# Optimization experiments

Hardware: AMD Instinct MI355X
Metric: run time of the kernel (lower is better)

The kernel has to match this reference:

```python
import jax, jax.numpy as jnp
import numpy as np

WS, SS, P, H = 7, 3, 14, 12  # window, shift, patch grid, heads
NW = (P // WS) ** 2          # windows per image = 4
N_WIN = WS * WS              # tokens per window = 49

def _rel_pos_index():
    coords = np.stack(np.meshgrid(np.arange(WS), np.arange(WS), indexing='ij')).reshape(2, -1)
    rel = (coords[:, :, None] - coords[:, None, :]).transpose(1, 2, 0).astype(np.int64)
    rel[..., 0] += WS - 1
    rel[..., 1] += WS - 1
    rel[..., 0] *= 2 * WS - 1
    return rel.sum(-1)  # [49,49]

def _shift_mask():
    img = np.zeros((P, P))
    sl = (slice(0, -WS), slice(-WS, -SS), slice(-SS, None))
    cnt = 0
    for h in sl:
        for w in sl:
            img[h, w] = cnt
            cnt += 1
    mw = img.reshape(P // WS, WS, P // WS, WS).transpose(0, 2, 1, 3).reshape(-1, N_WIN)
    am = mw[:, None, :] - mw[:, :, None]
    return np.where(am != 0, -100.0, 0.0).astype(np.float32)  # [nW,49,49]

RPI = jnp.asarray(_rel_pos_index())
MASK = jnp.asarray(_shift_mask())

def _hswish(x):
    return x * jnp.clip(x + 3.0, 0.0, 6.0) / 6.0

def _hsig(x):
    return jnp.clip(x + 3.0, 0.0, 6.0) / 6.0

def _bn(x, g, b, eps=1e-5):
    # training-mode batchnorm over (B,H,W) per channel, biased variance
    m = x.mean((0, 2, 3), keepdims=True)
    v = ((x - m) ** 2).mean((0, 2, 3), keepdims=True)
    return (x - m) / jnp.sqrt(v + eps) * g[None, :, None, None] + b[None, :, None, None]

def setup_inputs() -> dict:
    key = jax.random.key(0)
    ks = jax.random.split(key, 20)
    C, HID = 768, 3072
    return {
        'x': jax.random.normal(ks[0], (32, 197, C), jnp.float32),
        'w_qkv': jax.random.normal(ks[1], (3 * C, C), jnp.float32) * 0.02,
        'w_proj': jax.random.normal(ks[2], (C, C), jnp.float32) * 0.02,
        'b_proj': jax.random.normal(ks[3], (C,), jnp.float32) * 0.02,
        'rpb_table': jax.random.normal(ks[4], ((2 * WS - 1) ** 2, H), jnp.float32) * 0.02,
        'pw1_w': jax.random.normal(ks[5], (HID, C), jnp.float32) * 0.02,
        'bn1_g': 1.0 + jax.random.normal(ks[6], (HID,), jnp.float32) * 0.02,
        'bn1_b': jax.random.normal(ks[7], (HID,), jnp.float32) * 0.02,
        'dw_w': jax.random.normal(ks[8], (HID, 3, 3), jnp.float32) * 0.1,
        'bn2_g': 1.0 + jax.random.normal(ks[9], (HID,), jnp.float32) * 0.02,
        'bn2_b': jax.random.normal(ks[10], (HID,), jnp.float32) * 0.02,
        'se_w1': jax.random.normal(ks[11], (HID // 4, HID), jnp.float32) * 0.02,
        'se_b1': jax.random.normal(ks[12], (HID // 4,), jnp.float32) * 0.02,
        'se_w2': jax.random.normal(ks[13], (HID, HID // 4), jnp.float32) * 0.02,
        'se_b2': jax.random.normal(ks[14], (HID,), jnp.float32) * 0.02,
        'pw2_w': jax.random.normal(ks[15], (C, HID), jnp.float32) * 0.02,
        'bn3_g': 1.0 + jax.random.normal(ks[16], (C,), jnp.float32) * 0.02,
        'bn3_b': jax.random.normal(ks[17], (C,), jnp.float32) * 0.02,
    }

def reference(x, w_qkv, w_proj, b_proj, rpb_table, pw1_w, bn1_g, bn1_b, dw_w,
              bn2_g, bn2_b, se_w1, se_b1, se_w2, se_b2, pw2_w, bn3_g, bn3_b):
    B, N, C = x.shape
    hd = C // H
    scale = hd ** -0.5
    nw = P // WS

    cls_tok = x[:, :1]
    xs = x[:, 1:].reshape(B, P, P, C)
    xs = jnp.roll(xs, (-SS, -SS), axis=(1, 2))  # cyclic shift
    # window partition -> [B*nW, 49, C]
    win = xs.reshape(B, nw, WS, nw, WS, C).transpose(0, 1, 3, 2, 4, 5).reshape(B * NW, N_WIN, C)

    qkv = (win @ w_qkv.T).reshape(B * NW, N_WIN, 3, H, hd).transpose(2, 0, 3, 1, 4)
    q, k, v = qkv[0], qkv[1], qkv[2]  # [B*nW, H, 49, hd]
    attn = jnp.einsum('bhqd,bhkd->bhqk', q, k) * scale
    # relative position bias gather: [H,49,49]
    bias = rpb_table[RPI.reshape(-1)].reshape(N_WIN, N_WIN, H).transpose(2, 0, 1)
    attn = attn + bias[None]
    # shifted-window mask add
    attn = (attn.reshape(B, NW, H, N_WIN, N_WIN) + MASK[None, :, None]).reshape(B * NW, H, N_WIN, N_WIN)
    attn = jax.nn.softmax(attn, axis=-1)
    out = jnp.einsum('bhqk,bhkd->bhqd', attn, v).transpose(0, 2, 1, 3).reshape(B * NW, N_WIN, C)
    out = out @ w_proj.T + b_proj

    # window reverse + reverse shift
    xs = out.reshape(B, nw, nw, WS, WS, C).transpose(0, 1, 3, 2, 4, 5).reshape(B, P, P, C)
    xs = jnp.roll(xs, (SS, SS), axis=(1, 2))
    x = jnp.concatenate([cls_tok, xs.reshape(B, P * P, C)], axis=1)

    # LocalityFeedForward (inverted residual conv MLP with SE)
    cls_tok, xt = x[:, :1], x[:, 1:]
    f = xt.transpose(0, 2, 1).reshape(B, C, P, P)
    h = _hswish(_bn(jnp.einsum('bchw,oc->bohw', f, pw1_w), bn1_g, bn1_b))
    h = _hswish(_bn(jax.lax.conv_general_dilated(
        h, dw_w[:, None], (1, 1), 'SAME',
        feature_group_count=h.shape[1],
        dimension_numbers=('NCHW', 'OIHW', 'NCHW')), bn2_g, bn2_b))
    s = h.mean((2, 3))  # global avg pool [B, hid]
    s = _hsig(jax.nn.relu(s @ se_w1.T + se_b1) @ se_w2.T + se_b2)
    h = h * s[:, :, None, None]
    h = _bn(jnp.einsum('bchw,oc->bohw', h, pw2_w), bn3_g, bn3_b)
    f = f + h
    x = jnp.concatenate([cls_tok, f.reshape(B, C, P * P).transpose(0, 2, 1)], axis=1)
    return x
```

## Files before the change

### kernel.cpp

```cpp
#include <hip/hip_runtime.h>
#include <hip/hip_bf16.h>

typedef unsigned short ushort_t;
typedef unsigned int uint_t;
typedef short short8 __attribute__((ext_vector_type(8)));
typedef float floatx4 __attribute__((ext_vector_type(4)));

__device__ inline float b2f(ushort_t u){
    uint_t v = ((uint_t)u) << 16;
    return __uint_as_float(v);
}
__device__ inline ushort_t f2b(float f){
    uint_t v = __float_as_uint(f);
    uint_t r = (v + 0x7FFFu + ((v >> 16) & 1u)) >> 16;
    return (ushort_t)r;
}
__device__ inline void unpack8(uint4 u, float* f){
    uint_t w[4] = {u.x, u.y, u.z, u.w};
    #pragma unroll
    for (int i = 0; i < 4; ++i){
        f[2*i]   = __uint_as_float(w[i] << 16);
        f[2*i+1] = __uint_as_float(w[i] & 0xFFFF0000u);
    }
}
__device__ inline uint4 pack8(const float* f){
    uint4 o;
    uint_t w[4];
    #pragma unroll
    for (int i = 0; i < 4; ++i)
        w[i] = (uint_t)f2b(f[2*i]) | ((uint_t)f2b(f[2*i+1]) << 16);
    o.x = w[0]; o.y = w[1]; o.z = w[2]; o.w = w[3];
    return o;
}
__device__ inline ushort4 cvt4(float4 v){
    ushort4 o;
    o.x = f2b(v.x); o.y = f2b(v.y); o.z = f2b(v.z); o.w = f2b(v.w);
    return o;
}
__device__ inline float hswish(float y){
    return y * fminf(fmaxf(y + 3.f, 0.f), 6.f) * (1.f/6.f);
}

#define MROWS 6272
#define CDIM  768
#define HID   3072
#define QKV3  2304

__device__ inline int scatter_row(int ri){
    int w  = ri / 49, t = ri % 49;
    int b  = w >> 2,  wi = w & 3;
    int wy = wi >> 1, wx = wi & 1;
    int ty = t / 7,   tx = t % 7;
    int yd = (wy*7 + ty + 3) % 14;
    int xd = (wx*7 + tx + 3) % 14;
    return b*196 + yd*14 + xd;
}

__global__ __launch_bounds__(256) void cvt_f2b(const float4* __restrict__ in,
                                               ushort4* __restrict__ out, int n4){
    int i = blockIdx.x * 256 + threadIdx.x;
    if (i < n4) out[i] = cvt4(in[i]);
}

__global__ __launch_bounds__(256) void dw_transpose(const float* __restrict__ w,
                                                    float* __restrict__ wT){
    int i = blockIdx.x*256 + threadIdx.x;
    if (i < HID*9){ int c = i/9, k = i%9; wT[k*HID + c] = w[i]; }
}

__global__ __launch_bounds__(256) void gather_win(const float4* __restrict__ x,
                                                  ushort4* __restrict__ win){
    int idx = blockIdx.x * 256 + threadIdx.x;
    if (idx >= MROWS * 192) return;
    int r  = idx / 192, c4 = idx % 192;
    int w  = r / 49,  t  = r % 49;
    int b  = w >> 2,  wi = w & 3;
    int wy = wi >> 1, wx = wi & 1;
    int ty = t / 7,   tx = t % 7;
    int ys = (wy*7 + ty + 3) % 14;
    int xs = (wx*7 + tx + 3) % 14;
    win[idx] = cvt4(x[(size_t)b*197*192 + (size_t)(1 + ys*14 + xs)*192 + c4]);
}

__global__ __launch_bounds__(256) void gemm_bt(const ushort_t* __restrict__ A,
                                               const ushort_t* __restrict__ B,
                                               ushort_t* __restrict__ Cb,
                                               float* __restrict__ Cf,
                                               int M, int N, int K,
                                               const float* __restrict__ bias,
                                               float* __restrict__ stats,
                                               int scat){
    const int nx   = gridDim.x;
    int flat = blockIdx.y * nx + blockIdx.x;
    int xcd  = flat & 7;
    int k    = flat >> 3;
    int by   = xcd + 8 * (k / nx);
    int bx   = k % nx;
    if (by * 128 >= M) return;

    __shared__ __align__(16) ushort_t As[2][128*32];
    __shared__ __align__(16) ushort_t Bs[2][128*32];
    const int tid  = threadIdx.x;
    const int lane = tid & 63;
    const int wid  = tid >> 6;
    const int m0 = by * 128;
    const int n0 = bx * 128;
    const int wm = (wid >> 1) * 64;
    const int wn = (wid & 1) * 64;

    const int srow = (lane >> 2);
    const int scol = (lane & 3) * 8;

    floatx4 acc[4][4] = {};

    auto stage = [&](int buf, int k0){
        #pragma unroll
        for (int j = 0; j < 2; ++j){
            int ch  = wid*2 + j;
            const ushort_t* gA = A + (size_t)(m0 + ch*16 + srow)*K + k0 + scol;
            const ushort_t* gB = B + (size_t)(n0 + ch*16 + srow)*K + k0 + scol;
            __builtin_amdgcn_global_load_lds(
                (const __attribute__((address_space(1))) void*)gA,
                (__attribute__((address_space(3))) void*)(&As[buf][ch*512 + lane*8]), 16, 0, 0);
            __builtin_amdgcn_global_load_lds(
                (const __attribute__((address_space(1))) void*)gB,
                (__attribute__((address_space(3))) void*)(&Bs[buf][ch*512 + lane*8]), 16, 0, 0);
        }
    };

    stage(0, 0);
    __syncthreads();

    int cur = 0;
    const int fr = lane & 15;
    const int co = (lane >> 4) * 8;
    for (int k0 = 0; k0 < K; k0 += 32){
        if (k0 + 32 < K) stage(cur ^ 1, k0 + 32);

        short8 af[4], bfr[4];
        #pragma unroll
        for (int i = 0; i < 4; ++i){
            af[i]  = *(const short8*)(&As[cur][(wm + i*16 + fr)*32 + co]);
            bfr[i] = *(const short8*)(&Bs[cur][(wn + i*16 + fr)*32 + co]);
        }
        #pragma unroll
        for (int i = 0; i < 4; ++i)
            #pragma unroll
            for (int j = 0; j < 4; ++j)
                acc[i][j] = __builtin_amdgcn_mfma_f32_16x16x32_bf16(af[i], bfr[j], acc[i][j], 0, 0, 0);

        __syncthreads();
        cur ^= 1;
    }

    #pragma unroll
    for (int i = 0; i < 4; ++i){
        int grow = m0 + wm + i*16 + (lane >> 4)*4;
        #pragma unroll
        for (int j = 0; j < 4; ++j){
            int gcol = n0 + wn + j*16 + (lane & 15);
            float bv = bias ? bias[gcol] : 0.f;
            if (scat){
                #pragma unroll
                for (int r = 0; r < 4; ++r){
                    float v = acc[i][j][r] + bv;
                    size_t off = (size_t)scatter_row(grow + r)*N + gcol;
                    Cf[off] = v;
                    Cb[off] = f2b(v);
                }
            } else if (Cb){
                #pragma unroll
                for (int r = 0; r < 4; ++r)
                    Cb[(size_t)(grow + r)*N + gcol] = f2b(acc[i][j][r] + bv);
            } else {
                #pragma unroll
                for (int r = 0; r < 4; ++r)
                    Cf[(size_t)(grow + r)*N + gcol] = acc[i][j][r] + bv;
            }
        }
    }

    if (stats){
        #pragma unroll
        for (int j = 0; j < 4; ++j){
            int gcol = n0 + wn + j*16 + (lane & 15);
            float bv = bias ? bias[gcol] : 0.f;
            float sv = 0.f, sq = 0.f;
            #pragma unroll
            for (int i = 0; i < 4; ++i)
                #pragma unroll
                for (int r = 0; r < 4; ++r){
                    float v = acc[i][j][r] + bv;
                    sv += v; sq += v*v;
                }
            sv += __shfl_xor(sv, 16, 64);  sq += __shfl_xor(sq, 16, 64);
            sv += __shfl_xor(sv, 32, 64);  sq += __shfl_xor(sq, 32, 64);
            if (lane < 16){
                atomicAdd(&stats[gcol], sv);
                atomicAdd(&stats[N + gcol], sq);
            }
        }
    }
}

__global__ __launch_bounds__(256) void gemm_bt64(const ushort_t* __restrict__ A,
                                                 const ushort_t* __restrict__ B,
                                                 ushort_t* __restrict__ Cb,
                                                 float* __restrict__ Cf,
                                                 int M, int N, int K,
                                                 const float* __restrict__ bias,
                                                 float* __restrict__ stats,
                                                 int scat){
    const int nx   = gridDim.x;
    int flat = blockIdx.y * nx + blockIdx.x;
    int xcd  = flat & 7;
    int k    = flat >> 3;
    int by   = xcd + 8 * (k / nx);
    int bx   = k % nx;
    if (by * 128 >= M) return;

    __shared__ __align__(16) ushort_t As[2][128*32];
    __shared__ __align__(16) ushort_t Bs[2][64*32];
    const int tid  = threadIdx.x;
    const int lane = tid & 63;
    const int wid  = tid >> 6;
    const int m0 = by * 128;
    const int n0 = bx * 64;
    const int wm = (wid >> 1) * 64;
    const int wn = (wid & 1) * 32;

    const int srow = (lane >> 2);
    const int scol = (lane & 3) * 8;

    floatx4 acc[4][2] = {};

    auto stage = [&](int buf, int k0){
        #pragma unroll
        for (int j = 0; j < 2; ++j){
            int ch = wid*2 + j;
            const ushort_t* gA = A + (size_t)(m0 + ch*16 + srow)*K + k0 + scol;
            __builtin_amdgcn_global_load_lds(
                (const __attribute__((address_space(1))) void*)gA,
                (__attribute__((address_space(3))) void*)(&As[buf][ch*512 + lane*8]), 16, 0, 0);
        }
        const ushort_t* gB = B + (size_t)(n0 + wid*16 + srow)*K + k0 + scol;
        __builtin_amdgcn_global_load_lds(
            (const __attribute__((address_space(1))) void*)gB,
            (__attribute__((address_space(3))) void*)(&Bs[buf][wid*512 + lane*8]), 16, 0, 0);
    };

    stage(0, 0);
    __syncthreads();

    int cur = 0;
    const int fr = lane & 15;
    const int co = (lane >> 4) * 8;
    for (int k0 = 0; k0 < K; k0 += 32){
        if (k0 + 32 < K) stage(cur ^ 1, k0 + 32);

        short8 af[4], bfr[2];
        #pragma unroll
        for (int i = 0; i < 4; ++i)
            af[i]  = *(const short8*)(&As[cur][(wm + i*16 + fr)*32 + co]);
        #pragma unroll
        for (int j = 0; j < 2; ++j)
            bfr[j] = *(const short8*)(&Bs[cur][(wn + j*16 + fr)*32 + co]);
        #pragma unroll
        for (int i = 0; i < 4; ++i)
            #pragma unroll
            for (int j = 0; j < 2; ++j)
                acc[i][j] = __builtin_amdgcn_mfma_f32_16x16x32_bf16(af[i], bfr[j], acc[i][j], 0, 0, 0);

        __syncthreads();
        cur ^= 1;
    }

    #pragma unroll
    for (int i = 0; i < 4; ++i){
        int grow = m0 + wm + i*16 + (lane >> 4)*4;
        #pragma unroll
        for (int j = 0; j < 2; ++j){
            int gcol = n0 + wn + j*16 + (lane & 15);
            float bv = bias ? bias[gcol] : 0.f;
            if (scat){
                #pragma unroll
                for (int r = 0; r < 4; ++r){
                    float v = acc[i][j][r] + bv;
                    size_t off = (size_t)scatter_row(grow + r)*N + gcol;
                    Cf[off] = v;
                    Cb[off] = f2b(v);
                }
            } else if (Cb){
                #pragma unroll
                for (int r = 0; r < 4; ++r)
                    Cb[(size_t)(grow + r)*N + gcol] = f2b(acc[i][j][r] + bv);
            } else {
                #pragma unroll
                for (int r = 0; r < 4; ++r)
                    Cf[(size_t)(grow + r)*N + gcol] = acc[i][j][r] + bv;
            }
        }
    }

    if (stats){
        #pragma unroll
        for (int j = 0; j < 2; ++j){
            int gcol = n0 + wn + j*16 + (lane & 15);
            float bv = bias ? bias[gcol] : 0.f;
            float sv = 0.f, sq = 0.f;
            #pragma unroll
            for (int i = 0; i < 4; ++i)
                #pragma unroll
                for (int r = 0; r < 4; ++r){
                    float v = acc[i][j][r] + bv;
                    sv += v; sq += v*v;
                }
            sv += __shfl_xor(sv, 16, 64);  sq += __shfl_xor(sq, 16, 64);
            sv += __shfl_xor(sv, 32, 64);  sq += __shfl_xor(sq, 32, 64);
            if (lane < 16){
                atomicAdd(&stats[gcol], sv);
                atomicAdd(&stats[N + gcol], sq);
            }
        }
    }
}

__global__ __launch_bounds__(256) void bm_precompute(const float* __restrict__ rpb,
                                                     float* __restrict__ bm){
    int idx = blockIdx.x*256 + threadIdx.x;
    if (idx >= 12*4*64*64) return;
    int ki = idx & 63, qi = (idx >> 6) & 63, wi = (idx >> 12) & 3, h = idx >> 14;
    float v = -1e30f;
    if (qi < 49 && ki < 49){
        int qy = qi/7, qx = qi%7, ky = ki/7, kx = ki%7;
        int ridx = (qy - ky + 6)*13 + (qx - kx + 6);
        v = rpb[ridx*12 + h];
        int wy = wi >> 1, wx = wi & 1;
        int gqy = wy*7 + qy, gqx = wx*7 + qx, gky = wy*7 + ky, gkx = wx*7 + kx;
        int cq = ((gqy < 7) ? 0 : (gqy < 11 ? 1 : 2))*3 + ((gqx < 7) ? 0 : (gqx < 11 ? 1 : 2));
        int ck = ((gky < 7) ? 0 : (gky < 11 ? 1 : 2))*3 + ((gkx < 7) ? 0 : (gkx < 11 ? 1 : 2));
        if (cq != ck) v -= 100.f;
    }
    bm[idx] = v;
}

__global__ __launch_bounds__(256) void attn_mfma(const ushort_t* __restrict__ qkv,
                                                 ushort_t* __restrict__ outp,
                                                 const float* __restrict__ bm){
    __shared__ __align__(16) ushort_t Ps[64*72];
    __shared__ __align__(16) ushort_t VT[64*72];
    const int tid = threadIdx.x, lane = tid & 63, wid = tid >> 6;
    const int h = blockIdx.x, w = blockIdx.y, wi = w & 3;
    const int fr = lane & 15, quad = lane >> 4, co = quad*8;

    for (int idx = tid; idx < 64*64; idx += 256){
        int k = idx >> 6, n = idx & 63;
        ushort_t v = 0;
        if (k < 49) v = qkv[(size_t)(w*49 + k)*QKV3 + 1536 + h*64 + n];
        VT[n*72 + k] = v;
    }
    __syncthreads();

    floatx4 accs[4] = {};
    const ushort_t* qbase = qkv + (size_t)(w*49 + wid*16 + fr)*QKV3 + h*64;
    #pragma unroll
    for (int k0 = 0; k0 < 64; k0 += 32){
        short8 af = *(const short8*)(qbase + k0 + co);
        #pragma unroll
        for (int j = 0; j < 4; ++j){
            const ushort_t* kbase = qkv + (size_t)(w*49 + j*16 + fr)*QKV3 + 768 + h*64;
            short8 bf = *(const short8*)(kbase + k0 + co);
            accs[j] = __builtin_amdgcn_mfma_f32_16x16x32_bf16(af, bf, accs[j], 0, 0, 0);
        }
    }

    const float* bmh = bm + (size_t)((h*4 + wi)*64 + wid*16)*64;
    #pragma unroll
    for (int r = 0; r < 4; ++r){
        int lrow = quad*4 + r;
        float m = -3e38f;
        #pragma unroll
        for (int j = 0; j < 4; ++j){
            float a = accs[j][r]*0.125f + bmh[lrow*64 + j*16 + fr];
            accs[j][r] = a;
            m = fmaxf(m, a);
        }
        #pragma unroll
        for (int off = 1; off < 16; off <<= 1) m = fmaxf(m, __shfl_xor(m, off, 64));
        float s = 0.f;
        #pragma unroll
        for (int j = 0; j < 4; ++j){
            float e = __expf(accs[j][r] - m);
            accs[j][r] = e; s += e;
        }
        #pragma unroll
        for (int off = 1; off < 16; off <<= 1) s += __shfl_xor(s, off, 64);
        float inv = 1.f / s;
        #pragma unroll
        for (int j = 0; j < 4; ++j)
            Ps[(wid*16 + lrow)*72 + j*16 + fr] = f2b(accs[j][r]*inv);
    }
    __syncthreads();

    floatx4 acco[4] = {};
    #pragma unroll
    for (int k0 = 0; k0 < 64; k0 += 32){
        short8 af = *(const short8*)(Ps + (wid*16 + fr)*72 + k0 + co);
        #pragma unroll
        for (int j = 0; j < 4; ++j){
            short8 bf = *(const short8*)(VT + (j*16 + fr)*72 + k0 + co);
            acco[j] = __builtin_amdgcn_mfma_f32_16x16x32_bf16(af, bf, acco[j], 0, 0, 0);
        }
    }
    #pragma unroll
    for (int r = 0; r < 4; ++r){
        int qi = wid*16 + quad*4 + r;
        if (qi < 49){
            #pragma unroll
            for (int j = 0; j < 4; ++j)
                outp[(size_t)(w*49 + qi)*CDIM + h*64 + j*16 + fr] = f2b(acco[j][r]);
        }
    }
}

__global__ void zero_f32(float* __restrict__ p, int n){
    int i = blockIdx.x*256 + threadIdx.x;
    if (i < n) p[i] = 0.f;
}
__global__ __launch_bounds__(256) void bn_stats_v(const ushort_t* __restrict__ X,
                                                  float* __restrict__ sums){
    const int cgl = threadIdx.x & 31;
    const int rp  = threadIdx.x >> 5;
    const int cg  = blockIdx.x*32 + cgl;
    const int r0  = blockIdx.y*224;
    const uint4* Xb = (const uint4*)X;
    float s[8] = {}, q[8] = {};
    for (int r = r0 + rp; r < r0 + 224; r += 8){
        uint4 u = Xb[(size_t)r*384 + cg];
        float f[8]; unpack8(u, f);
        #pragma unroll
        for (int e = 0; e < 8; ++e){ s[e] += f[e]; q[e] += f[e]*f[e]; }
    }
    #pragma unroll
    for (int e = 0; e < 8; ++e){
        s[e] += __shfl_xor(s[e], 32, 64);
        q[e] += __shfl_xor(q[e], 32, 64);
    }
    __shared__ float red[4][32][17];
    const int wv = threadIdx.x >> 6;
    if ((threadIdx.x & 32) == 0){
        #pragma unroll
        for (int e = 0; e < 8; ++e){
            red[wv][cgl][e]   = s[e];
            red[wv][cgl][8+e] = q[e];
        }
    }
    __syncthreads();
    #pragma unroll
    for (int k = 0; k < 2; ++k){
        int o = threadIdx.x*2 + k;
        int cgo = o >> 4, e = o & 15;
        float v = red[0][cgo][e] + red[1][cgo][e] + red[2][cgo][e] + red[3][cgo][e];
        int c = blockIdx.x*256 + cgo*8 + (e & 7);
        atomicAdd(&sums[(e < 8 ? 0 : HID) + c], v);
    }
}
__global__ void bn_finalize(float* __restrict__ sums, const float* __restrict__ g,
                            const float* __restrict__ b, int Cch){
    int c = blockIdx.x*256 + threadIdx.x;
    if (c >= Cch) return;
    float mean = sums[c] * (1.f/6272.f);
    float var  = sums[Cch + c] * (1.f/6272.f) - mean*mean;
    float sc = g[c] * rsqrtf(var + 1e-5f);
    sums[c] = sc;
    sums[Cch + c] = b[c] - mean*sc;
}

__global__ __launch_bounds__(256) void dwconv_v(const ushort_t* __restrict__ in,
                                                const float* __restrict__ wT,
                                                const float* __restrict__ ss,
                                                ushort_t* __restrict__ out){
    int idx = blockIdx.x*256 + threadIdx.x;
    if (idx >= MROWS*384) return;
    int r  = idx / 384, cg = idx % 384;
    int b  = r / 196,  p  = r % 196;
    int y  = p / 14,   x  = p % 14;
    int c  = cg*8;
    const uint4* inb = (const uint4*)(in + (size_t)b*196*HID);
    float sc[8], sh[8];
    {
        const float4* s0 = (const float4*)(ss + c);
        const float4* s1 = (const float4*)(ss + HID + c);
        float4 a0 = s0[0], a1 = s0[1], b0 = s1[0], b1 = s1[1];
        sc[0]=a0.x; sc[1]=a0.y; sc[2]=a0.z; sc[3]=a0.w;
        sc[4]=a1.x; sc[5]=a1.y; sc[6]=a1.z; sc[7]=a1.w;
        sh[0]=b0.x; sh[1]=b0.y; sh[2]=b0.z; sh[3]=b0.w;
        sh[4]=b1.x; sh[5]=b1.y; sh[6]=b1.z; sh[7]=b1.w;
    }
    float acc[8] = {};
    #pragma unroll
    for (int ky = 0; ky < 3; ++ky){
        int yy = y + ky - 1;
        if ((unsigned)yy >= 14u) continue;
        #pragma unroll
        for (int kx = 0; kx < 3; ++kx){
            int xx = x + kx - 1;
            if ((unsigned)xx >= 14u) continue;
            uint4 u = inb[(yy*14 + xx)*384 + cg];
            float fin[8]; unpack8(u, fin);
            const float4* wp = (const float4*)(wT + (ky*3 + kx)*HID + c);
            float4 w0 = wp[0], w1 = wp[1];
            float wv[8] = {w0.x,w0.y,w0.z,w0.w,w1.x,w1.y,w1.z,w1.w};
            #pragma unroll
            for (int e = 0; e < 8; ++e)
                acc[e] += hswish(fin[e]*sc[e] + sh[e]) * wv[e];
        }
    }
    ((uint4*)out)[idx] = pack8(acc);
}

__global__ __launch_bounds__(256) void se_mean_v(const ushort_t* __restrict__ X,
                                                 const float* __restrict__ ss,
                                                 float* __restrict__ s){
    const int b   = blockIdx.x;
    const int cgl = threadIdx.x & 31;
    const int rp  = threadIdx.x >> 5;
    const int cg  = blockIdx.y*32 + cgl;
    const int c   = cg*8;
    float sc[8], sh[8];
    #pragma unroll
    for (int e = 0; e < 8; ++e){ sc[e] = ss[c+e]; sh[e] = ss[HID+c+e]; }
    const uint4* Xb = (const uint4*)(X + (size_t)b*196*HID);
    float a[8] = {};
    for (int p = rp; p < 196; p += 8){
        uint4 u = Xb[(size_t)p*384 + cg];
        float f[8]; unpack8(u, f);
        #pragma unroll
        for (int e = 0; e < 8; ++e) a[e] += hswish(f[e]*sc[e] + sh[e]);
    }
    #pragma unroll
    for (int e = 0; e < 8; ++e) a[e] += __shfl_xor(a[e], 32, 64);
    __shared__ float red[4][32][9];
    const int wv = threadIdx.x >> 6;
    if ((threadIdx.x & 32) == 0){
        #pragma unroll
        for (int e = 0; e < 8; ++e) red[wv][cgl][e] = a[e];
    }
    __syncthreads();
    {
        int o = threadIdx.x;
        int cgo = o >> 3, e = o & 7;
        float v = red[0][cgo][e] + red[1][cgo][e] + red[2][cgo][e] + red[3][cgo][e];
        s[(size_t)b*HID + blockIdx.y*256 + cgo*8 + e] = v * (1.f/196.f);
    }
}
__global__ __launch_bounds__(256) void se_fc(const float* __restrict__ in,
                                             const float* __restrict__ w,
                                             const float* __restrict__ bias,
                                             float* __restrict__ out,
                                             int IN, int OUT, int mode){
    int wv   = (blockIdx.x*256 + threadIdx.x) >> 6;
    int lane = threadIdx.x & 63;
    if (wv >= OUT) return;
    const float* wr = w + (size_t)wv * IN;
    float acc[32];
    #pragma unroll
    for (int b = 0; b < 32; ++b) acc[b] = 0.f;
    for (int k = lane; k < IN; k += 64){
        float wval = wr[k];
        #pragma unroll
        for (int b = 0; b < 32; ++b)
            acc[b] += in[b*IN + k] * wval;
    }
    #pragma unroll
    for (int b = 0; b < 32; ++b){
        float v = acc[b];
        #pragma unroll
        for (int off = 32; off; off >>= 1) v += __shfl_down(v, off, 64);
        if (lane == 0){
            float a = v + bias[wv];
            if (mode == 0) a = fmaxf(a, 0.f);
            else           a = fminf(fmaxf(a + 3.f, 0.f), 6.f) * (1.f/6.f);
            out[b*OUT + wv] = a;
        }
    }
}
__global__ __launch_bounds__(256) void se_scale(ushort_t* __restrict__ X,
                                                const float* __restrict__ ss,
                                                const float* __restrict__ s2){
    int idx = blockIdx.x*256 + threadIdx.x;
    if (idx >= MROWS * (HID/8)) return;
    int r = idx / (HID/8), c8 = idx % (HID/8);
    int b = r / 196;
    int c = c8*8;
    uint4 u = ((uint4*)X)[idx];
    float f[8]; unpack8(u, f);
    const float* sp = s2 + b*HID + c;
    #pragma unroll
    for (int e = 0; e < 8; ++e)
        f[e] = hswish(f[e]*ss[c+e] + ss[HID+c+e]) * sp[e];
    ((uint4*)X)[idx] = pack8(f);
}

__global__ __launch_bounds__(256) void final_k(const float4* __restrict__ xin,
                                               const float4* __restrict__ f,
                                               const float4* __restrict__ h4,
                                               const float* __restrict__ ss,
                                               float4* __restrict__ outp){
    int idx = blockIdx.x*256 + threadIdx.x;
    if (idx >= 32*197*192) return;
    int b = idx / (197*192);
    int rem = idx % (197*192);
    int n = rem / 192, c4 = rem % 192;
    if (n == 0){ outp[idx] = xin[idx]; return; }
    size_t off = ((size_t)b*196 + n - 1)*192 + c4;
    float4 hv = h4[off];
    float4 fv = f[off];
    float4 o;
    int c = c4*4;
    o.x = fv.x + hv.x*ss[c+0] + ss[CDIM + c+0];
    o.y = fv.y + hv.y*ss[c+1] + ss[CDIM + c+1];
    o.z = fv.z + hv.z*ss[c+2] + ss[CDIM + c+2];
    o.w = fv.w + hv.w*ss[c+3] + ss[CDIM + c+3];
    outp[idx] = o;
}

extern "C" void kernel_launch(void* const* d_in, const int* in_sizes, int n_in,
                              void* d_out, int out_size, void* d_ws, size_t ws_size,
                              hipStream_t stream){
    const float* x      = (const float*)d_in[0];
    const float* w_qkv  = (const float*)d_in[1];
    const float* w_proj = (const float*)d_in[2];
    const float* b_proj = (const float*)d_in[3];
    const float* rpb    = (const float*)d_in[4];
    const float* pw1_w  = (const float*)d_in[5];
    const float* bn1_g  = (const float*)d_in[6];
    const float* bn1_b  = (const float*)d_in[7];
    const float* dw_w   = (const float*)d_in[8];
    const float* bn2_g  = (const float*)d_in[9];
    const float* bn2_b  = (const float*)d_in[10];
    const float* se_w1  = (const float*)d_in[11];
    const float* se_b1  = (const float*)d_in[12];
    const float* se_w2  = (const float*)d_in[13];
    const float* se_b2  = (const float*)d_in[14];
    const float* pw2_w  = (const float*)d_in[15];
    const float* bn3_g  = (const float*)d_in[16];
    const float* bn3_b  = (const float*)d_in[17];

    char* ws = (char*)d_ws;
    ushort_t* win    = (ushort_t*)(ws + 0);
    float*    bm     = (float*)(ws + 0);
    ushort_t* qkv    = (ushort_t*)(ws + 9633792);
    ushort_t* fbf    = (ushort_t*)(ws + 0);
    ushort_t* pw1b   = (ushort_t*)(ws + 9633792);
    ushort_t* hb     = (ushort_t*)(ws + 0);
    ushort_t* wqkvb  = (ushort_t*)(ws + 38535168);
    ushort_t* attnb  = (ushort_t*)(ws + 38535168);
    ushort_t* wprojb = (ushort_t*)(ws + 48168960);
    ushort_t* ha     = (ushort_t*)(ws + 38535168);
    float*    h4     = (float*)(ws + 38535168);
    ushort_t* pw2b   = (ushort_t*)(ws + 57802752);
    float*    f      = (float*)(ws + 77070336);
    float*    stats  = (float*)(ws + 96337920);
    float*    s      = (float*)(ws + 96362496);
    float*    s1     = (float*)(ws + 96755712);
    float*    s2     = (float*)(ws + 96854016);
    float*    dwwT   = (float*)(ws + 96854016);

    const int vec_rows = (MROWS*192 + 255)/256;
    const int vec_hid8 = (MROWS*(HID/8) + 255)/256;
    const int GY = 56;

    dw_transpose<<<(HID*9 + 255)/256, 256, 0, stream>>>(dw_w, dwwT);
    cvt_f2b<<<(QKV3*CDIM/4 + 255)/256, 256, 0, stream>>>((const float4*)w_qkv, (ushort4*)wqkvb, QKV3*CDIM/4);
    cvt_f2b<<<(CDIM*CDIM/4 + 255)/256, 256, 0, stream>>>((const float4*)w_proj, (ushort4*)wprojb, CDIM*CDIM/4);

    gather_win<<<vec_rows, 256, 0, stream>>>((const float4*)x, (ushort4*)win);
    gemm_bt<<<dim3(QKV3/128, GY), 256, 0, stream>>>(win, wqkvb, qkv, nullptr, MROWS, QKV3, CDIM, nullptr, nullptr, 0);
    bm_precompute<<<(12*4*64*64)/256, 256, 0, stream>>>(rpb, bm);
    attn_mfma<<<dim3(12, 128), 256, 0, stream>>>(qkv, attnb, bm);
    cvt_f2b<<<(HID*CDIM/4 + 255)/256, 256, 0, stream>>>((const float4*)pw1_w, (ushort4*)pw1b, HID*CDIM/4);
    zero_f32<<<24, 256, 0, stream>>>(stats, 2*HID);
    gemm_bt64<<<dim3(CDIM/64, GY), 256, 0, stream>>>(attnb, wprojb, fbf, f, MROWS, CDIM, CDIM, b_proj, nullptr, 1);

    gemm_bt<<<dim3(HID/128, GY), 256, 0, stream>>>(fbf, pw1b, ha, nullptr, MROWS, HID, CDIM, nullptr, stats, 0);
    bn_finalize<<<HID/256, 256, 0, stream>>>(stats, bn1_g, bn1_b, HID);

    dwconv_v<<<(MROWS*384 + 255)/256, 256, 0, stream>>>(ha, dwwT, stats, hb);
    cvt_f2b<<<(CDIM*HID/4 + 255)/256, 256, 0, stream>>>((const float4*)pw2_w, (ushort4*)pw2b, CDIM*HID/4);
    zero_f32<<<24, 256, 0, stream>>>(stats, 2*HID);
    bn_stats_v<<<dim3(12, 28), 256, 0, stream>>>(hb, stats);
    bn_finalize<<<HID/256, 256, 0, stream>>>(stats, bn2_g, bn2_b, HID);

    se_mean_v<<<dim3(32, 12), 256, 0, stream>>>(hb, stats, s);
    se_fc<<<dim3((CDIM*64)/256), 256, 0, stream>>>(s, se_w1, se_b1, s1, HID, CDIM, 0);
    se_fc<<<dim3((HID*64)/256), 256, 0, stream>>>(s1, se_w2, se_b2, s2, CDIM, HID, 1);
    se_scale<<<vec_hid8, 256, 0, stream>>>(hb, stats, s2);

    zero_f32<<<6, 256, 0, stream>>>(stats, 2*CDIM);
    gemm_bt64<<<dim3(CDIM/64, GY), 256, 0, stream>>>(hb, pw2b, nullptr, h4, MROWS, CDIM, HID, nullptr, stats, 0);
    bn_finalize<<<CDIM/256, 256, 0, stream>>>(stats, bn3_g, bn3_b, CDIM);
    final_k<<<(32*197*192 + 255)/256, 256, 0, stream>>>((const float4*)x, (const float4*)f, (const float4*)h4, stats, (float4*)d_out);
}
```

Baseline: 544.4 us.

## Triple-buffer GEMM LDS staging with vmcnt waits and one barrier per k-step

```diff
diff --git a/kernel.cpp b/kernel.cpp
--- a/kernel.cpp
+++ b/kernel.cpp
@@ -98,8 +98,8 @@
     int bx   = k % nx;
     if (by * 128 >= M) return;
 
-    __shared__ __align__(16) ushort_t As[2][128*32];
-    __shared__ __align__(16) ushort_t Bs[2][128*32];
+    __shared__ __align__(16) ushort_t As[3][128*32];
+    __shared__ __align__(16) ushort_t Bs[3][128*32];
     const int tid  = threadIdx.x;
     const int lane = tid & 63;
     const int wid  = tid >> 6;
@@ -128,14 +128,18 @@
         }
     };
 
+    const int NK = K >> 5;
     stage(0, 0);
-    __syncthreads();
-
-    int cur = 0;
+    stage(1, 32);
+
     const int fr = lane & 15;
     const int co = (lane >> 4) * 8;
-    for (int k0 = 0; k0 < K; k0 += 32){
-        if (k0 + 32 < K) stage(cur ^ 1, k0 + 32);
+    int cur = 0;
+    for (int it = 0; it < NK; ++it){
+        if (it < NK - 1) asm volatile("s_waitcnt vmcnt(4)" ::: "memory");
+        else             asm volatile("s_waitcnt vmcnt(0)" ::: "memory");
+        __builtin_amdgcn_s_barrier();
+        __builtin_amdgcn_sched_barrier(0);
 
         short8 af[4], bfr[4];
         #pragma unroll
@@ -149,8 +153,11 @@
             for (int j = 0; j < 4; ++j)
                 acc[i][j] = __builtin_amdgcn_mfma_f32_16x16x32_bf16(af[i], bfr[j], acc[i][j], 0, 0, 0);
 
-        __syncthreads();
-        cur ^= 1;
+        if (it + 2 < NK){
+            int nb = cur + 2; if (nb >= 3) nb -= 3;
+            stage(nb, (it + 2) << 5);
+        }
+        cur = (cur == 2) ? 0 : cur + 1;
     }
 
     #pragma unroll
@@ -219,8 +226,8 @@
     int bx   = k % nx;
     if (by * 128 >= M) return;
 
-    __shared__ __align__(16) ushort_t As[2][128*32];
-    __shared__ __align__(16) ushort_t Bs[2][64*32];
+    __shared__ __align__(16) ushort_t As[3][128*32];
+    __shared__ __align__(16) ushort_t Bs[3][64*32];
     const int tid  = threadIdx.x;
     const int lane = tid & 63;
     const int wid  = tid >> 6;
@@ -249,14 +256,18 @@
             (__attribute__((address_space(3))) void*)(&Bs[buf][wid*512 + lane*8]), 16, 0, 0);
     };
 
+    const int NK = K >> 5;
     stage(0, 0);
-    __syncthreads();
-
-    int cur = 0;
+    stage(1, 32);
+
     const int fr = lane & 15;
     const int co = (lane >> 4) * 8;
-    for (int k0 = 0; k0 < K; k0 += 32){
-        if (k0 + 32 < K) stage(cur ^ 1, k0 + 32);
+    int cur = 0;
+    for (int it = 0; it < NK; ++it){
+        if (it < NK - 1) asm volatile("s_waitcnt vmcnt(3)" ::: "memory");
+        else             asm volatile("s_waitcnt vmcnt(0)" ::: "memory");
+        __builtin_amdgcn_s_barrier();
+        __builtin_amdgcn_sched_barrier(0);
 
         short8 af[4], bfr[2];
         #pragma unroll
@@ -271,8 +282,11 @@
             for (int j = 0; j < 2; ++j)
                 acc[i][j] = __builtin_amdgcn_mfma_f32_16x16x32_bf16(af[i], bfr[j], acc[i][j], 0, 0, 0);
 
-        __syncthreads();
-        cur ^= 1;
+        if (it + 2 < NK){
+            int nb = cur + 2; if (nb >= 3) nb -= 3;
+            stage(nb, (it + 2) << 5);
+        }
+        cur = (cur == 2) ? 0 : cur + 1;
     }
 
     #pragma unroll
```

New measurement: 539.8 us. About the same (-0.9%).

## Swizzle LDS tiles and use fine-grained vmcnt waits in GEMM kernels

Applied to the files above, without the earlier changes.

```diff
diff --git a/kernel.cpp b/kernel.cpp
--- a/kernel.cpp
+++ b/kernel.cpp
@@ -109,7 +109,7 @@
     const int wn = (wid & 1) * 64;
 
     const int srow = (lane >> 2);
-    const int scol = (lane & 3) * 8;
+    const int scol = (((lane & 3) ^ ((lane >> 3) & 3)) * 8);
 
     floatx4 acc[4][4] = {};
 
@@ -128,28 +128,36 @@
         }
     };
 
+    const int NK = K >> 5;
     stage(0, 0);
-    __syncthreads();
-
+
+    const int fr   = lane & 15;
+    const int quad = lane >> 4;
+    const int cosw = (quad ^ ((fr >> 1) & 3)) * 8;
     int cur = 0;
-    const int fr = lane & 15;
-    const int co = (lane >> 4) * 8;
-    for (int k0 = 0; k0 < K; k0 += 32){
-        if (k0 + 32 < K) stage(cur ^ 1, k0 + 32);
+    for (int it = 0; it < NK; ++it){
+        __builtin_amdgcn_sched_barrier(0);
+        __builtin_amdgcn_s_barrier();
+        if (it + 1 < NK){
+            stage(cur ^ 1, (it + 1) << 5);
+            asm volatile("s_waitcnt vmcnt(4)" ::: "memory");
+        } else {
+            asm volatile("s_waitcnt vmcnt(0)" ::: "memory");
+        }
+        __builtin_amdgcn_s_barrier();
+        __builtin_amdgcn_sched_barrier(0);
 
         short8 af[4], bfr[4];
         #pragma unroll
         for (int i = 0; i < 4; ++i){
-            af[i]  = *(const short8*)(&As[cur][(wm + i*16 + fr)*32 + co]);
-            bfr[i] = *(const short8*)(&Bs[cur][(wn + i*16 + fr)*32 + co]);
+            af[i]  = *(const short8*)(&As[cur][(wm + i*16 + fr)*32 + cosw]);
+            bfr[i] = *(const short8*)(&Bs[cur][(wn + i*16 + fr)*32 + cosw]);
         }
         #pragma unroll
         for (int i = 0; i < 4; ++i)
             #pragma unroll
             for (int j = 0; j < 4; ++j)
                 acc[i][j] = __builtin_amdgcn_mfma_f32_16x16x32_bf16(af[i], bfr[j], acc[i][j], 0, 0, 0);
-
-        __syncthreads();
         cur ^= 1;
     }
 
@@ -230,7 +238,7 @@
     const int wn = (wid & 1) * 32;
 
     const int srow = (lane >> 2);
-    const int scol = (lane & 3) * 8;
+    const int scol = (((lane & 3) ^ ((lane >> 3) & 3)) * 8);
 
     floatx4 acc[4][2] = {};
 
@@ -249,29 +257,37 @@
             (__attribute__((address_space(3))) void*)(&Bs[buf][wid*512 + lane*8]), 16, 0, 0);
     };
 
+    const int NK = K >> 5;
     stage(0, 0);
-    __syncthreads();
-
+
+    const int fr   = lane & 15;
+    const int quad = lane >> 4;
+    const int cosw = (quad ^ ((fr >> 1) & 3)) * 8;
     int cur = 0;
-    const int fr = lane & 15;
-    const int co = (lane >> 4) * 8;
-    for (int k0 = 0; k0 < K; k0 += 32){
-        if (k0 + 32 < K) stage(cur ^ 1, k0 + 32);
+    for (int it = 0; it < NK; ++it){
+        __builtin_amdgcn_sched_barrier(0);
+        __builtin_amdgcn_s_barrier();
+        if (it + 1 < NK){
+            stage(cur ^ 1, (it + 1) << 5);
+            asm volatile("s_waitcnt vmcnt(3)" ::: "memory");
+        } else {
+            asm volatile("s_waitcnt vmcnt(0)" ::: "memory");
+        }
+        __builtin_amdgcn_s_barrier();
+        __builtin_amdgcn_sched_barrier(0);
 
         short8 af[4], bfr[2];
         #pragma unroll
         for (int i = 0; i < 4; ++i)
-            af[i]  = *(const short8*)(&As[cur][(wm + i*16 + fr)*32 + co]);
+            af[i]  = *(const short8*)(&As[cur][(wm + i*16 + fr)*32 + cosw]);
         #pragma unroll
         for (int j = 0; j < 2; ++j)
-            bfr[j] = *(const short8*)(&Bs[cur][(wn + j*16 + fr)*32 + co]);
+            bfr[j] = *(const short8*)(&Bs[cur][(wn + j*16 + fr)*32 + cosw]);
         #pragma unroll
         for (int i = 0; i < 4; ++i)
             #pragma unroll
             for (int j = 0; j < 2; ++j)
                 acc[i][j] = __builtin_amdgcn_mfma_f32_16x16x32_bf16(af[i], bfr[j], acc[i][j], 0, 0, 0);
-
-        __syncthreads();
         cur ^= 1;
     }
 
```

Result: no change. 542.2 us (-0.4%).
